# Performance work log

Measured on AMD Instinct MI355X. Metric: run time of the kernel, lower is better.

Reference implementation:

```python
import jax, jax.numpy as jnp
import numpy as np

H = 1024   # hidden_size
A = 16     # number_ab (branches)
O = 4      # num_outputs per branch
B = 4096   # batch
P = 2048   # number of selected rows
EPS = 1e-5


def setup_inputs() -> dict:
    key = jax.random.key(0)
    ks = jax.random.split(key, 12)
    s = 0.02  # weight init scale
    inp = {
        "X": jax.random.normal(ks[0], (B, H), jnp.float32),
        "X1": jax.random.normal(ks[1], (B, H), jnp.float32),
        # stacked per-branch parameters (batched over antibody axis A)
        "W1": jax.random.normal(ks[2], (A, H, H), jnp.float32) * s,
        "b1": jnp.zeros((A, H), jnp.float32),
        "W2": jax.random.normal(ks[3], (A, H, H), jnp.float32) * s,
        "b2": jnp.zeros((A, H), jnp.float32),
        "W3": jax.random.normal(ks[4], (A, H, H), jnp.float32) * s,
        "b3": jnp.zeros((A, H), jnp.float32),
        "gamma": jnp.ones((A, H), jnp.float32),
        "beta": jnp.zeros((A, H), jnp.float32),
        "W4": jax.random.normal(ks[5], (A, H, O), jnp.float32) * s,
        "b4": jnp.zeros((A, O), jnp.float32),
        "positions_y": jax.random.randint(ks[6], (P,), 0, B, jnp.int32),
    }
    return inp


def reference(X, X1, W1, b1, W2, b2, W3, b3, gamma, beta, W4, b4, positions_y):
    # z = l1(X) + l2(X1) per branch, batched over A: [B, A, H]
    z = (jnp.einsum('bh,aho->bao', X, W1) + b1
         + jnp.einsum('bh,aho->bao', X1, W2) + b2)
    # mlm: Linear -> ReLU -> LayerNorm -> Linear
    h = jax.nn.relu(jnp.einsum('bah,aho->bao', z, W3) + b3)  # [B, A, H]
    mu = jnp.mean(h, axis=-1, keepdims=True)
    var = jnp.var(h, axis=-1, keepdims=True)  # biased, matches nn.LayerNorm
    hn = (h - mu) / jnp.sqrt(var + EPS) * gamma + beta
    y = jnp.einsum('bah,aho->bao', hn, W4) + b4  # [B, A, O]
    # torch.cat along dim 1 over branches -> [B, A*O]
    Y = y.reshape(B, A * O)
    return Y[positions_y]
```

## Files before the change

kernel.cpp:

```cpp
#include <hip/hip_runtime.h>
#include <hip/hip_bf16.h>

using bf16 = __hip_bfloat16;
typedef __bf16 v8bf __attribute__((ext_vector_type(8)));
typedef float v4f __attribute__((ext_vector_type(4)));

#define H_ 1024
#define A_ 16
#define O_ 4
#define B_ 4096
#define P_ 2048
#define EPS_ 1e-5f

__device__ __forceinline__ void gl_lds16(const void* g, void* l) {
    __builtin_amdgcn_global_load_lds(
        (const __attribute__((address_space(1))) void*)g,
        (__attribute__((address_space(3))) void*)l, 16, 0, 0);
}

__global__ __launch_bounds__(256) void gather_bias_k(const float* __restrict__ X,
                                                     const float* __restrict__ X1,
                                                     const int* __restrict__ pos,
                                                     bf16* __restrict__ XX,
                                                     const float* __restrict__ b1,
                                                     const float* __restrict__ b2,
                                                     float* __restrict__ b12) {
    if (blockIdx.x >= P_) {
        int i = (blockIdx.x - P_) * 256 + threadIdx.x;
        if (i < A_ * H_) b12[i] = b1[i] + b2[i];
        return;
    }
    int p = blockIdx.x;
    int row = pos[p];
    const float4* x  = (const float4*)(X  + (size_t)row * H_);
    const float4* x1 = (const float4*)(X1 + (size_t)row * H_);
    bf16* o = XX + (size_t)p * (2 * H_);
    int i = threadIdx.x;
    float4 v = x[i];
    __align__(8) bf16 t[4];
    t[0] = __float2bfloat16(v.x); t[1] = __float2bfloat16(v.y);
    t[2] = __float2bfloat16(v.z); t[3] = __float2bfloat16(v.w);
    *(uint2*)(o + i * 4) = *(const uint2*)t;
    float4 w = x1[i];
    t[0] = __float2bfloat16(w.x); t[1] = __float2bfloat16(w.y);
    t[2] = __float2bfloat16(w.z); t[3] = __float2bfloat16(w.w);
    *(uint2*)(o + H_ + i * 4) = *(const uint2*)t;
}

__global__ __launch_bounds__(256) void transpose_k(const float* __restrict__ W1s,
                                                   const float* __restrict__ W2s,
                                                   const float* __restrict__ W3s,
                                                   bf16* __restrict__ WT12,
                                                   bf16* __restrict__ WT3) {
    __shared__ float tile[64][65];
    const int which = blockIdx.z >> 4;
    const int a = blockIdx.z & 15;
    const float* src = (which == 0) ? W1s : (which == 1) ? W2s : W3s;

    const int k0 = blockIdx.x * 64;
    const int n0 = blockIdx.y * 64;
    const float* s = src + (size_t)a * H_ * H_;
    const int tc = threadIdx.x & 15;
    const int tr = threadIdx.x >> 4;
#pragma unroll
    for (int r = 0; r < 64; r += 16) {
        float4 v = *(const float4*)(s + (size_t)(k0 + tr + r) * H_ + n0 + tc * 4);
        tile[tr + r][tc * 4 + 0] = v.x;
        tile[tr + r][tc * 4 + 1] = v.y;
        tile[tr + r][tc * 4 + 2] = v.z;
        tile[tr + r][tc * 4 + 3] = v.w;
    }
    __syncthreads();
    bf16* d;
    int ldK;
    if (which < 2) {
        d = WT12 + (size_t)a * H_ * (2 * H_) + which * H_;
        ldK = 2 * H_;
    } else {
        d = WT3 + (size_t)a * H_ * H_;
        ldK = H_;
    }
    const int wc = threadIdx.x & 7;
    const int wr = threadIdx.x >> 3;
#pragma unroll
    for (int r = 0; r < 64; r += 32) {
        const int n = wr + r;
        __align__(16) bf16 tmp[8];
#pragma unroll
        for (int j = 0; j < 8; j++) tmp[j] = __float2bfloat16(tile[wc * 8 + j][n]);
        *(uint4*)(d + (size_t)(n0 + n) * ldK + k0 + wc * 8) = *(const uint4*)tmp;
    }
}

template <bool RELU>
__global__ __launch_bounds__(512) void gemm_bt(const bf16* __restrict__ Amat, size_t aStrideA,
                                               const bf16* __restrict__ Bt,
                                               const float* __restrict__ bias,
                                               bf16* __restrict__ C,
                                               int M, int N, int K) {
    __shared__ __align__(16) char smem[131072];

    const int L = blockIdx.x;
    const int xcd = L & 7;
    const int g = L >> 3;
    const int bm = g & 7;
    const int bna = xcd + 8 * (g >> 3);
    const int bn = bna & 3;
    const int a = bna >> 2;

    const bf16* Ab = Amat + (size_t)a * aStrideA;
    const bf16* Bb = Bt + (size_t)a * (size_t)N * K;

    const int tid = threadIdx.x;
    const int lane = tid & 63;
    const int w = tid >> 6;
    const int lr = lane & 15;
    const int q = lane >> 4;
    const int wm = (w >> 2) * 128;
    const int wn = (w & 3) * 64;

    const int swz = lr & 7;
    const int aRd0 = (wm + lr) * 128 + ((q ^ swz) << 4);
    const int aRd1 = (wm + lr) * 128 + (((q + 4) ^ swz) << 4);
    const int bRd0 = (wn + lr) * 128 + ((q ^ swz) << 4);
    const int bRd1 = (wn + lr) * 128 + (((q + 4) ^ swz) << 4);

    const int sr = lane >> 3;
    const int sc = (lane & 7) ^ sr;
    const size_t k8 = (size_t)8 * K;
    const bf16* aSt = Ab + (size_t)(bm * 256 + w * 32 + sr) * K + sc * 8;
    const bf16* bSt = Bb + (size_t)(bn * 256 + w * 32 + sr) * K + sc * 8;
    char* AsL = smem + w * 4096;
    char* BsL = smem + 65536 + w * 4096;

    v4f acc[8][4];
#pragma unroll
    for (int i = 0; i < 8; i++)
#pragma unroll
        for (int j = 0; j < 4; j++) acc[i][j] = (v4f){0.f, 0.f, 0.f, 0.f};

    const int nk = K / 64;

#define STAGE(tt, bo)                                    \
    {                                                    \
        const bf16* as_ = aSt + (size_t)(tt) * 64;       \
        const bf16* bs_ = bSt + (size_t)(tt) * 64;       \
        gl_lds16(as_,            AsL + (bo));            \
        gl_lds16(as_ + k8,       AsL + (bo) + 1024);     \
        gl_lds16(as_ + 2 * k8,   AsL + (bo) + 2048);     \
        gl_lds16(as_ + 3 * k8,   AsL + (bo) + 3072);     \
        gl_lds16(bs_,            BsL + (bo));            \
        gl_lds16(bs_ + k8,       BsL + (bo) + 1024);     \
        gl_lds16(bs_ + 2 * k8,   BsL + (bo) + 2048);     \
        gl_lds16(bs_ + 3 * k8,   BsL + (bo) + 3072);     \
    }

    STAGE(0, 0);

    for (int t = 0; t < nk; ++t) {
        const int bo = (t & 1) << 15;
        asm volatile("s_waitcnt vmcnt(0)" ::: "memory");
        __syncthreads();
        if (t + 1 < nk) STAGE(t + 1, bo ^ 32768);

        const char* Ar = smem + bo;
        const char* Br = smem + 65536 + bo;

        v8bf b0[4], b1[4], af[4];

#pragma unroll
        for (int ni = 0; ni < 4; ni++) b0[ni] = *(const v8bf*)(Br + bRd0 + ni * 2048);
#pragma unroll
        for (int mi = 0; mi < 4; mi++) af[mi] = *(const v8bf*)(Ar + aRd0 + mi * 2048);
        __builtin_amdgcn_s_setprio(1);
#pragma unroll
        for (int mi = 0; mi < 4; mi++)
#pragma unroll
            for (int ni = 0; ni < 4; ni++)
                acc[mi][ni] = __builtin_amdgcn_mfma_f32_16x16x32_bf16(af[mi], b0[ni],
                                                                      acc[mi][ni], 0, 0, 0);
        __builtin_amdgcn_s_setprio(0);
        __builtin_amdgcn_s_barrier();

#pragma unroll
        for (int mi = 0; mi < 4; mi++) af[mi] = *(const v8bf*)(Ar + aRd0 + (mi + 4) * 2048);
        __builtin_amdgcn_s_setprio(1);
#pragma unroll
        for (int mi = 0; mi < 4; mi++)
#pragma unroll
            for (int ni = 0; ni < 4; ni++)
                acc[mi + 4][ni] = __builtin_amdgcn_mfma_f32_16x16x32_bf16(af[mi], b0[ni],
                                                                          acc[mi + 4][ni], 0, 0, 0);
        __builtin_amdgcn_s_setprio(0);
        __builtin_amdgcn_s_barrier();

#pragma unroll
        for (int ni = 0; ni < 4; ni++) b1[ni] = *(const v8bf*)(Br + bRd1 + ni * 2048);
#pragma unroll
        for (int mi = 0; mi < 4; mi++) af[mi] = *(const v8bf*)(Ar + aRd1 + mi * 2048);
        __builtin_amdgcn_s_setprio(1);
#pragma unroll
        for (int mi = 0; mi < 4; mi++)
#pragma unroll
            for (int ni = 0; ni < 4; ni++)
                acc[mi][ni] = __builtin_amdgcn_mfma_f32_16x16x32_bf16(af[mi], b1[ni],
                                                                      acc[mi][ni], 0, 0, 0);
        __builtin_amdgcn_s_setprio(0);
        __builtin_amdgcn_s_barrier();

#pragma unroll
        for (int mi = 0; mi < 4; mi++) af[mi] = *(const v8bf*)(Ar + aRd1 + (mi + 4) * 2048);
        __builtin_amdgcn_s_setprio(1);
#pragma unroll
        for (int mi = 0; mi < 4; mi++)
#pragma unroll
            for (int ni = 0; ni < 4; ni++)
                acc[mi + 4][ni] = __builtin_amdgcn_mfma_f32_16x16x32_bf16(af[mi], b1[ni],
                                                                          acc[mi + 4][ni], 0, 0, 0);
        __builtin_amdgcn_s_setprio(0);
    }
#undef STAGE

    bf16* Cb = C + (size_t)a * (size_t)M * N;
#pragma unroll
    for (int ni = 0; ni < 4; ni++) {
        const int col = bn * 256 + wn + ni * 16 + lr;
        const float bv = bias[(size_t)a * N + col];
#pragma unroll
        for (int mi = 0; mi < 8; mi++) {
            const int row0 = bm * 256 + wm + mi * 16 + q * 4;
#pragma unroll
            for (int rg = 0; rg < 4; rg++) {
                float v = acc[mi][ni][rg] + bv;
                if (RELU) v = v > 0.f ? v : 0.f;
                Cb[(size_t)(row0 + rg) * N + col] = __float2bfloat16(v);
            }
        }
    }
}

__global__ __launch_bounds__(256) void ln_head_k(const bf16* __restrict__ Hb,
                                                 const float* __restrict__ gamma,
                                                 const float* __restrict__ beta,
                                                 const float* __restrict__ W4,
                                                 const float* __restrict__ b4,
                                                 float* __restrict__ out) {
    const int w = blockIdx.x * 4 + (threadIdx.x >> 6);
    const int lane = threadIdx.x & 63;
    const int a = w >> 9;
    const int p0 = (w & 511) * 4;
    const float* g = gamma + (size_t)a * H_;
    const float* be = beta + (size_t)a * H_;
    const float4* w4 = (const float4*)(W4 + (size_t)a * H_ * O_);

    float gv[16], bv[16];
    float4 wv[16];
#pragma unroll
    for (int half = 0; half < 2; half++) {
        const int kb = half * 512 + lane * 8;
        const float4 g4a = *(const float4*)(g + kb);
        const float4 g4b = *(const float4*)(g + kb + 4);
        const float4 b4a = *(const float4*)(be + kb);
        const float4 b4b = *(const float4*)(be + kb + 4);
        gv[half * 8 + 0] = g4a.x; gv[half * 8 + 1] = g4a.y;
        gv[half * 8 + 2] = g4a.z; gv[half * 8 + 3] = g4a.w;
        gv[half * 8 + 4] = g4b.x; gv[half * 8 + 5] = g4b.y;
        gv[half * 8 + 6] = g4b.z; gv[half * 8 + 7] = g4b.w;
        bv[half * 8 + 0] = b4a.x; bv[half * 8 + 1] = b4a.y;
        bv[half * 8 + 2] = b4a.z; bv[half * 8 + 3] = b4a.w;
        bv[half * 8 + 4] = b4b.x; bv[half * 8 + 5] = b4b.y;
        bv[half * 8 + 6] = b4b.z; bv[half * 8 + 7] = b4b.w;
#pragma unroll
        for (int j = 0; j < 8; j++) wv[half * 8 + j] = w4[kb + j];
    }
    const float bo = b4[a * O_ + (lane & 3)];

    for (int rr = 0; rr < 4; rr++) {
        const int p = p0 + rr;
        const bf16* hrow = Hb + ((size_t)a * P_ + p) * H_;
        v8bf h0 = *(const v8bf*)(hrow + lane * 8);
        v8bf h1 = *(const v8bf*)(hrow + 512 + lane * 8);
        float hv[16];
        float s = 0.f, ss = 0.f;
#pragma unroll
        for (int j = 0; j < 8; j++) {
            float v = (float)h0[j];
            hv[j] = v; s += v; ss += v * v;
        }
#pragma unroll
        for (int j = 0; j < 8; j++) {
            float v = (float)h1[j];
            hv[8 + j] = v; s += v; ss += v * v;
        }
#pragma unroll
        for (int off = 32; off; off >>= 1) {
            s += __shfl_xor(s, off);
            ss += __shfl_xor(ss, off);
        }
        const float mu = s * (1.f / H_);
        const float var = ss * (1.f / H_) - mu * mu;
        const float rstd = rsqrtf(var + EPS_);
        float a0 = 0.f, a1 = 0.f, a2 = 0.f, a3 = 0.f;
#pragma unroll
        for (int j = 0; j < 16; j++) {
            const float hn = (hv[j] - mu) * rstd * gv[j] + bv[j];
            a0 += hn * wv[j].x;
            a1 += hn * wv[j].y;
            a2 += hn * wv[j].z;
            a3 += hn * wv[j].w;
        }
#pragma unroll
        for (int off = 32; off; off >>= 1) {
            a0 += __shfl_xor(a0, off);
            a1 += __shfl_xor(a1, off);
            a2 += __shfl_xor(a2, off);
            a3 += __shfl_xor(a3, off);
        }
        if (lane < 4) {
            const float v = (lane == 0 ? a0 : lane == 1 ? a1 : lane == 2 ? a2 : a3) + bo;
            out[(size_t)p * (A_ * O_) + a * O_ + lane] = v;
        }
    }
}

extern "C" void kernel_launch(void* const* d_in, const int* in_sizes, int n_in,
                              void* d_out, int out_size, void* d_ws, size_t ws_size,
                              hipStream_t stream) {
    const float* X     = (const float*)d_in[0];
    const float* X1    = (const float*)d_in[1];
    const float* W1    = (const float*)d_in[2];
    const float* b1    = (const float*)d_in[3];
    const float* W2    = (const float*)d_in[4];
    const float* b2    = (const float*)d_in[5];
    const float* W3    = (const float*)d_in[6];
    const float* b3    = (const float*)d_in[7];
    const float* gamma = (const float*)d_in[8];
    const float* beta  = (const float*)d_in[9];
    const float* W4    = (const float*)d_in[10];
    const float* b4    = (const float*)d_in[11];
    const int* pos     = (const int*)d_in[12];
    float* out = (float*)d_out;

    char* ws = (char*)d_ws;
    bf16* XX   = (bf16*)(ws);
    bf16* Z    = (bf16*)(ws + ((size_t)8 << 20));
    bf16* WT3  = (bf16*)(ws + ((size_t)72 << 20));
    bf16* WT12 = (bf16*)(ws + ((size_t)104 << 20));
    float* b12 = (float*)(ws + ((size_t)168 << 20));
    bf16* Hb   = WT12;

    gather_bias_k<<<P_ + 64, 256, 0, stream>>>(X, X1, pos, XX, b1, b2, b12);
    dim3 tgrid(H_ / 64, H_ / 64, 3 * A_);
    transpose_k<<<tgrid, 256, 0, stream>>>(W1, W2, W3, WT12, WT3);

    gemm_bt<false><<<512, 512, 0, stream>>>(XX, 0, WT12, b12, Z, P_, H_, 2 * H_);
    gemm_bt<true><<<512, 512, 0, stream>>>(Z, (size_t)P_ * H_, WT3, b3, Hb, P_, H_, H_);

    ln_head_k<<<P_ * A_ / 16, 256, 0, stream>>>(Hb, gamma, beta, W4, b4, out);
}
```

Measured before the change: 477.6 us.

## Split K-tile into half-slabs and interleave async prefetch with MFMA phases

Restructures the GEMM main loop so each 64-wide K tile is stored as two 32-wide half slabs with a new 4-way XOR swizzle. Global-to-LDS prefetches for the next tile are spread across the four MFMA phases, and partial vmcnt waits replace the full drain at the top of each iteration. The goal is to hide global load latency behind compute and avoid the per-iteration stall. It adds barriers and fragile wait-count accounting, and the last-iteration vmcnt(4) wait may be inconsistent with the loads actually outstanding.

```diff
diff --git a/kernel.cpp b/kernel.cpp
--- a/kernel.cpp
+++ b/kernel.cpp
@@ -119,19 +119,17 @@
     const int wm = (w >> 2) * 128;
     const int wn = (w & 3) * 64;
 
-    const int swz = lr & 7;
-    const int aRd0 = (wm + lr) * 128 + ((q ^ swz) << 4);
-    const int aRd1 = (wm + lr) * 128 + (((q + 4) ^ swz) << 4);
-    const int bRd0 = (wn + lr) * 128 + ((q ^ swz) << 4);
-    const int bRd1 = (wn + lr) * 128 + (((q + 4) ^ swz) << 4);
-
-    const int sr = lane >> 3;
-    const int sc = (lane & 7) ^ sr;
-    const size_t k8 = (size_t)8 * K;
-    const bf16* aSt = Ab + (size_t)(bm * 256 + w * 32 + sr) * K + sc * 8;
-    const bf16* bSt = Bb + (size_t)(bn * 256 + w * 32 + sr) * K + sc * 8;
-    char* AsL = smem + w * 4096;
-    char* BsL = smem + 65536 + w * 4096;
+    const int swz = (lr >> 1) & 3;
+    const int aBase = (wm + lr) * 64 + ((q ^ swz) << 4);
+    const int bBase = (wn + lr) * 64 + ((q ^ swz) << 4);
+
+    const int grow = lane >> 2;
+    const int gch = ((lane & 3) ^ ((lane >> 3) & 3)) * 8;
+    const bf16* aG = Ab + (size_t)(bm * 256 + w * 32 + grow) * K + gch;
+    const bf16* bG = Bb + (size_t)(bn * 256 + w * 32 + grow) * K + gch;
+    const size_t k16 = (size_t)16 * K;
+    char* AsM = smem;
+    char* BsM = smem + 65536;
 
     v4f acc[8][4];
 #pragma unroll
@@ -141,97 +139,112 @@
 
     const int nk = K / 64;
 
-#define STAGE(tt, bo)                                    \
-    {                                                    \
-        const bf16* as_ = aSt + (size_t)(tt) * 64;       \
-        const bf16* bs_ = bSt + (size_t)(tt) * 64;       \
-        gl_lds16(as_,            AsL + (bo));            \
-        gl_lds16(as_ + k8,       AsL + (bo) + 1024);     \
-        gl_lds16(as_ + 2 * k8,   AsL + (bo) + 2048);     \
-        gl_lds16(as_ + 3 * k8,   AsL + (bo) + 3072);     \
-        gl_lds16(bs_,            BsL + (bo));            \
-        gl_lds16(bs_ + k8,       BsL + (bo) + 1024);     \
-        gl_lds16(bs_ + 2 * k8,   BsL + (bo) + 2048);     \
-        gl_lds16(bs_ + 3 * k8,   BsL + (bo) + 3072);     \
-    }
-
-    STAGE(0, 0);
+#define STG(gp, base, dd, ss, tt)                                              \
+    {                                                                          \
+        gl_lds16((gp) + (size_t)(tt) * 64 + (ss) * 32,                         \
+                 (base) + (dd) * 32768 + (ss) * 16384 + w * 2048);             \
+        gl_lds16((gp) + (size_t)(tt) * 64 + (ss) * 32 + k16,                   \
+                 (base) + (dd) * 32768 + (ss) * 16384 + w * 2048 + 1024);      \
+    }
+
+    STG(aG, AsM, 0, 0, 0)
+    STG(bG, BsM, 0, 0, 0)
+    STG(aG, AsM, 0, 1, 0)
+    STG(bG, BsM, 0, 1, 0)
+    asm volatile("s_waitcnt vmcnt(0)" ::: "memory");
+    __syncthreads();
 
     for (int t = 0; t < nk; ++t) {
-        const int bo = (t & 1) << 15;
-        asm volatile("s_waitcnt vmcnt(0)" ::: "memory");
-        __syncthreads();
-        if (t + 1 < nk) STAGE(t + 1, bo ^ 32768);
-
-        const char* Ar = smem + bo;
-        const char* Br = smem + 65536 + bo;
-
-        v8bf b0[4], b1[4], af[4];
-
-#pragma unroll
-        for (int ni = 0; ni < 4; ni++) b0[ni] = *(const v8bf*)(Br + bRd0 + ni * 2048);
-#pragma unroll
-        for (int mi = 0; mi < 4; mi++) af[mi] = *(const v8bf*)(Ar + aRd0 + mi * 2048);
+        const int d = t & 1, nd = d ^ 1;
+        const char* Ad = smem + d * 32768;
+        const char* Bd = smem + 65536 + d * 32768;
+        const bool pf = (t + 1 < nk);
+
+        v8bf av[4], bv[4];
+
+#pragma unroll
+        for (int ni = 0; ni < 4; ni++) bv[ni] = *(const v8bf*)(Bd + bBase + ni * 1024);
+#pragma unroll
+        for (int mi = 0; mi < 4; mi++) av[mi] = *(const v8bf*)(Ad + aBase + mi * 1024);
+        if (pf) STG(aG, AsM, nd, 0, t + 1)
+        __builtin_amdgcn_sched_barrier(0);
+        __builtin_amdgcn_s_barrier();
         __builtin_amdgcn_s_setprio(1);
 #pragma unroll
         for (int mi = 0; mi < 4; mi++)
 #pragma unroll
             for (int ni = 0; ni < 4; ni++)
-                acc[mi][ni] = __builtin_amdgcn_mfma_f32_16x16x32_bf16(af[mi], b0[ni],
+                acc[mi][ni] = __builtin_amdgcn_mfma_f32_16x16x32_bf16(av[mi], bv[ni],
                                                                       acc[mi][ni], 0, 0, 0);
         __builtin_amdgcn_s_setprio(0);
         __builtin_amdgcn_s_barrier();
 
 #pragma unroll
-        for (int mi = 0; mi < 4; mi++) af[mi] = *(const v8bf*)(Ar + aRd0 + (mi + 4) * 2048);
+        for (int mi = 0; mi < 4; mi++) av[mi] = *(const v8bf*)(Ad + aBase + (mi + 4) * 1024);
+        if (pf) STG(bG, BsM, nd, 0, t + 1)
+        __builtin_amdgcn_sched_barrier(0);
+        __builtin_amdgcn_s_barrier();
         __builtin_amdgcn_s_setprio(1);
 #pragma unroll
         for (int mi = 0; mi < 4; mi++)
 #pragma unroll
             for (int ni = 0; ni < 4; ni++)
-                acc[mi + 4][ni] = __builtin_amdgcn_mfma_f32_16x16x32_bf16(af[mi], b0[ni],
+                acc[mi + 4][ni] = __builtin_amdgcn_mfma_f32_16x16x32_bf16(av[mi], bv[ni],
                                                                           acc[mi + 4][ni], 0, 0, 0);
         __builtin_amdgcn_s_setprio(0);
-        __builtin_amdgcn_s_barrier();
-
-#pragma unroll
-        for (int ni = 0; ni < 4; ni++) b1[ni] = *(const v8bf*)(Br + bRd1 + ni * 2048);
-#pragma unroll
-        for (int mi = 0; mi < 4; mi++) af[mi] = *(const v8bf*)(Ar + aRd1 + mi * 2048);
+        if (pf) {
+            asm volatile("s_waitcnt vmcnt(4)" ::: "memory");
+        } else {
+            asm volatile("s_waitcnt vmcnt(0)" ::: "memory");
+        }
+        __builtin_amdgcn_s_barrier();
+
+#pragma unroll
+        for (int ni = 0; ni < 4; ni++) bv[ni] = *(const v8bf*)(Bd + 16384 + bBase + ni * 1024);
+#pragma unroll
+        for (int mi = 0; mi < 4; mi++) av[mi] = *(const v8bf*)(Ad + 16384 + aBase + mi * 1024);
+        if (pf) STG(aG, AsM, nd, 1, t + 1)
+        __builtin_amdgcn_sched_barrier(0);
+        __builtin_amdgcn_s_barrier();
         __builtin_amdgcn_s_setprio(1);
 #pragma unroll
         for (int mi = 0; mi < 4; mi++)
 #pragma unroll
             for (int ni = 0; ni < 4; ni++)
-                acc[mi][ni] = __builtin_amdgcn_mfma_f32_16x16x32_bf16(af[mi], b1[ni],
+                acc[mi][ni] = __builtin_amdgcn_mfma_f32_16x16x32_bf16(av[mi], bv[ni],
                                                                       acc[mi][ni], 0, 0, 0);
         __builtin_amdgcn_s_setprio(0);
         __builtin_amdgcn_s_barrier();
 
 #pragma unroll
-        for (int mi = 0; mi < 4; mi++) af[mi] = *(const v8bf*)(Ar + aRd1 + (mi + 4) * 2048);
+        for (int mi = 0; mi < 4; mi++) av[mi] = *(const v8bf*)(Ad + 16384 + aBase + (mi + 4) * 1024);
+        if (pf) STG(bG, BsM, nd, 1, t + 1)
+        __builtin_amdgcn_sched_barrier(0);
+        __builtin_amdgcn_s_barrier();
         __builtin_amdgcn_s_setprio(1);
 #pragma unroll
         for (int mi = 0; mi < 4; mi++)
 #pragma unroll
             for (int ni = 0; ni < 4; ni++)
-                acc[mi + 4][ni] = __builtin_amdgcn_mfma_f32_16x16x32_bf16(af[mi], b1[ni],
+                acc[mi + 4][ni] = __builtin_amdgcn_mfma_f32_16x16x32_bf16(av[mi], bv[ni],
                                                                           acc[mi + 4][ni], 0, 0, 0);
         __builtin_amdgcn_s_setprio(0);
-    }
-#undef STAGE
+        asm volatile("s_waitcnt vmcnt(4)" ::: "memory");
+        __builtin_amdgcn_s_barrier();
+    }
+#undef STG
 
     bf16* Cb = C + (size_t)a * (size_t)M * N;
 #pragma unroll
     for (int ni = 0; ni < 4; ni++) {
         const int col = bn * 256 + wn + ni * 16 + lr;
-        const float bv = bias[(size_t)a * N + col];
+        const float bv2 = bias[(size_t)a * N + col];
 #pragma unroll
         for (int mi = 0; mi < 8; mi++) {
             const int row0 = bm * 256 + wm + mi * 16 + q * 4;
 #pragma unroll
             for (int rg = 0; rg < 4; rg++) {
-                float v = acc[mi][ni][rg] + bv;
+                float v = acc[mi][ni][rg] + bv2;
                 if (RELU) v = v > 0.f ? v : 0.f;
                 Cb[(size_t)(row0 + rg) * N + col] = __float2bfloat16(v);
             }
```

After: 484.2 us. About the same (+1.4%).
